# Kernel tuning notes

Measured on AMD Instinct MI355X. Metric: run time of the kernel, lower is better.

## Reference

```python
import jax, jax.numpy as jnp
import numpy as np

B, S = 64, 512
VOCAB, D, H, NH = 50000, 256, 256, 4
MAX_DUR = 12.0
SCALE_RATE = 1.0


def setup_inputs() -> dict:
    key = jax.random.key(0)
    ks = jax.random.split(key, 12)
    s = 1.0 / np.sqrt(H)
    inp = {
        "src": jax.random.randint(ks[0], (B, S), 0, VOCAB),
        "input_len": jax.random.randint(ks[1], (B,), 1, S + 1),
        "fix_src": jax.random.uniform(ks[2], (B, S), jnp.float32) * MAX_DUR,
        "emb_table": jax.random.normal(ks[3], (VOCAB, D), jnp.float32) * 0.02,
        "Wi": jax.random.uniform(ks[4], (H, D), jnp.float32, -s, s),
        "bi": jax.random.uniform(ks[5], (H,), jnp.float32, -s, s),
        "Wh": jax.random.uniform(ks[6], (H, NH * H), jnp.float32, -s, s),
        "bh": jax.random.uniform(ks[7], (H,), jnp.float32, -s, s),
        "fc1_W": jax.random.uniform(ks[8], (D, NH * H), jnp.float32, -s, s),
        "fc1_b": jax.random.uniform(ks[9], (D,), jnp.float32, -s, s),
        "fc2_W": jax.random.uniform(ks[10], (2, D), jnp.float32, -s, s),
        "fc2_b": jax.random.uniform(ks[11], (2,), jnp.float32, -s, s),
    }
    return inp


def _forward(src, input_len, fix_src, emb_table, Wi, bi, Wh, bh, fc1_W, fc1_b, fc2_W, fc2_b):
    emb = emb_table[src]                      # [B, S, D]
    offsets = jnp.arange(NH, dtype=emb.dtype) * (MAX_DUR / NH)  # [NH]
    h0 = jnp.zeros((NH, B, H), emb.dtype)

    def step(h, xd):
        x, d = xd                             # x [B,D], d [B]
        hcat = jnp.swapaxes(h, 0, 1).reshape(B, NH * H)
        cand = jnp.tanh(x @ Wi.T + bi + hcat @ Wh.T + bh)        # [B,H]
        g = jax.nn.sigmoid(d[:, None] * SCALE_RATE - offsets)    # [B,NH]
        gt = g.T[:, :, None]                                     # [NH,B,1]
        h_new = gt * cand[None, :, :] + (1.0 - gt) * h           # [NH,B,H]
        out = jnp.swapaxes(h_new, 0, 1).reshape(B, NH * H)
        return h_new, out

    xs = (jnp.swapaxes(emb, 0, 1), fix_src.T)  # [S,B,D], [S,B]
    _, outs = jax.lax.scan(step, h0, xs)       # [S, B, NH*H]
    outs = jnp.swapaxes(outs, 0, 1)            # [B, S, NH*H]
    sel = outs[jnp.arange(B), input_len - 1]   # gather at last valid step, [B, NH*H]
    hid = jnp.tanh(sel @ fc1_W.T + fc1_b)      # [B, D]
    return hid @ fc2_W.T + fc2_b               # [B, 2]


def reference(src, input_len, fix_src, emb_table, Wi, bi, Wh, bh, fc1_W, fc1_b, fc2_W, fc2_b):
    return _forward(src, input_len, fix_src, emb_table, Wi, bi, Wh, bh, fc1_W, fc1_b, fc2_W, fc2_b)
```

## Files before the change

### kernel.cpp

```cpp
#include <hip/hip_runtime.h>
#include <stdint.h>

constexpr int BB = 64;
constexpr int SS = 512;
constexpr int DD = 256;
constexpr int HH = 256;
constexpr int NHH = 4;
constexpr int KK = 1024;

constexpr int TT = 512;

typedef _Float16 f16;
typedef _Float16 f16x2 __attribute__((ext_vector_type(2)));
typedef _Float16 half8 __attribute__((ext_vector_type(8)));
typedef float f32x4 __attribute__((ext_vector_type(4)));

__device__ inline float dot2p(uint32_t a, uint32_t b, float c) {
  f16x2 av = __builtin_bit_cast(f16x2, a);
  f16x2 bv = __builtin_bit_cast(f16x2, b);
#if defined(__has_builtin)
#if __has_builtin(__builtin_amdgcn_fdot2)
  return __builtin_amdgcn_fdot2(av, bv, c, false);
#else
  return c + (float)av.x * (float)bv.x + (float)av.y * (float)bv.y;
#endif
#else
  return c + (float)av.x * (float)bv.x + (float)av.y * (float)bv.y;
#endif
}

__device__ inline float dot8(uint4 w, uint4 a, float c) {
  c = dot2p(w.x, a.x, c);
  c = dot2p(w.y, a.y, c);
  c = dot2p(w.z, a.z, c);
  c = dot2p(w.w, a.w, c);
  return c;
}

__device__ inline uint32_t pack2(float a, float b) {
  f16x2 v;
  v.x = (f16)a;
  v.y = (f16)b;
  return __builtin_bit_cast(uint32_t, v);
}

__device__ inline float fast_tanh(float x) {
  x = fminf(fmaxf(x, -15.f), 15.f);
  float e = __expf(2.f * x);
  return 1.f - 2.f / (e + 1.f);
}

__device__ __host__ inline int chunk_of(int p, int wv) {
  if (wv == 0) return 2 * p;
  if (wv == 7) return 2 * p + 1;
  return (2 * p + 1 + wv) & 7;
}

__global__ __launch_bounds__(256) void k_prep(
    const float* __restrict__ Wh, uint4* __restrict__ Wq,
    const float* __restrict__ fc1_W, float* __restrict__ fc1T,
    const float* __restrict__ Wi, f16* __restrict__ wif) {
  __shared__ __align__(16) char sarena[16384];
  const int blk = blockIdx.x;
  const int t = threadIdx.x;
  if (blk < 32) {
    f16* lds = (f16*)sarena;
    const int p = blk >> 3, wv = blk & 7;
    const int cw = chunk_of(p, wv);
    {
      const int r = t >> 2, j = t & 3;
      const float* s = Wh + (size_t)(64 * p + r) * KK + 256 * j + 32 * cw;
      f16* d = lds + r * 128 + 32 * j;
#pragma unroll
      for (int i = 0; i < 32; i += 4) {
        float4 x = *(const float4*)(s + i);
        d[i] = (f16)x.x;
        d[i + 1] = (f16)x.y;
        d[i + 2] = (f16)x.z;
        d[i + 3] = (f16)x.w;
      }
    }
    __syncthreads();
    {
      const int mgrp = t >> 6, l = t & 63;
#pragma unroll
      for (int k2 = 0; k2 < 4; ++k2) {
        int mm = mgrp * 4 + k2;
        int j = mm >> 2, u = mm & 3;
        uint4 v = *(const uint4*)(lds + l * 128 + 32 * j + 8 * u);
        Wq[(size_t)(p * 16 + mm) * TT + wv * 64 + l] = v;
      }
    }
  } else if (blk < 288) {
    float* tile = (float*)sarena;
    const int tile_id = blk - 32;
    const int ti = tile_id >> 5, tj = tile_id & 31;
    const int lr = t >> 3, lc4 = t & 7;
    {
      float4 x = *(const float4*)(fc1_W + (size_t)(ti * 32 + lr) * 1024 +
                                  tj * 32 + 4 * lc4);
      float* d = tile + lr * 33 + 4 * lc4;
      d[0] = x.x;
      d[1] = x.y;
      d[2] = x.z;
      d[3] = x.w;
    }
    __syncthreads();
    {
      float4 o;
      o.x = tile[(4 * lc4 + 0) * 33 + lr];
      o.y = tile[(4 * lc4 + 1) * 33 + lr];
      o.z = tile[(4 * lc4 + 2) * 33 + lr];
      o.w = tile[(4 * lc4 + 3) * 33 + lr];
      *(float4*)(fc1T + (size_t)(tj * 32 + lr) * 256 + ti * 32 + 4 * lc4) = o;
    }
  } else {
    const int g4 = ((blk - 288) * 256 + t) * 4;
    float4 x = *(const float4*)(Wi + g4);
    uint2 dw;
    dw.x = pack2(x.x, x.y);
    dw.y = pack2(x.z, x.w);
    *(uint2*)(wif + g4) = dw;
  }
}

__global__ __launch_bounds__(256) void k_u_mfma(
    const int* __restrict__ src, const float* __restrict__ emb,
    const f16* __restrict__ wif, const float* __restrict__ bi,
    const float* __restrict__ bh, const int* __restrict__ input_len,
    f16* __restrict__ U) {
  __shared__ __align__(16) char xls[32768];
  const int row0 = blockIdx.x * 64;
  const int b = row0 >> 9;
  if ((row0 & 511) >= input_len[b]) return;
  const int t = threadIdx.x;
  const int w = t >> 6, l = t & 63;

  for (int rr = 0; rr < 16; ++rr) {
    int r = w * 16 + rr;
    int srcid = src[row0 + r];
    const float4 x = *(const float4*)(emb + (size_t)srcid * DD + l * 4);
    uint2 dw;
    dw.x = pack2(x.x, x.y);
    dw.y = pack2(x.z, x.w);
    int byte = (r * 512 + l * 8) ^ ((r & 7) << 4);
    *(uint2*)(xls + byte) = dw;
  }
  __syncthreads();

  const int lm = l & 15, lk = l >> 4;
  const int arow = w * 16 + lm;
  const int xs = (arow & 7) << 4;

  for (int ct = 0; ct < 16; ++ct) {
    const int o = ct * 16 + lm;
    f32x4 acc = {0.f, 0.f, 0.f, 0.f};
    const f16* bp = wif + (size_t)o * 256 + lk * 8;
#pragma unroll
    for (int kt = 0; kt < 8; ++kt) {
      int ab = (arow * 512 + kt * 64 + lk * 16) ^ xs;
      half8 af = *(const half8*)(xls + ab);
      half8 bf = *(const half8*)(bp + kt * 32);
      acc = __builtin_amdgcn_mfma_f32_16x16x32_f16(af, bf, acc, 0, 0, 0);
    }
    float bias = bi[o] + bh[o];
#pragma unroll
    for (int reg = 0; reg < 4; ++reg) {
      int grow = row0 + w * 16 + lk * 4 + reg;
      U[(size_t)grow * HH + o] = (f16)(acc[reg] + bias);
    }
  }
}

__global__ void __attribute__((amdgpu_flat_work_group_size(512, 512),
                               amdgpu_waves_per_eu(2, 2)))
k_recurrence(
    const uint4* __restrict__ Wq, const f16* __restrict__ U,
    const float* __restrict__ fix_src, const int* __restrict__ input_len,
    const float* __restrict__ fc1T, const float* __restrict__ fc1_b,
    const float* __restrict__ fc2_W, const float* __restrict__ fc2_b,
    float* __restrict__ out, uint32_t* __restrict__ Cex,
    float* __restrict__ FPg, int* __restrict__ Flg) {
  __shared__ __align__(16) char arena[61440];
  f16* cbufX = (f16*)arena;
  uint4* cvecX = (uint4*)arena;
  float* part = (float*)(arena + 512);
  float* partials = (float*)(arena + 512);
  float* hbuf = (float*)(arena + 16896);
  float* fsbuf = (float*)(arena + 17920);

  const int idx = blockIdx.x;
  const int b = idx & 63;
  const int p = idx >> 6;
  const int t = threadIdx.x;
  const int wv = t >> 6, l = t & 63;
  const int out_i = t & 255, ch2 = t >> 8;

  const int cw = chunk_of(p, wv);
  const int q = cw >> 1, half = cw & 1;

  uint4 w[16];
  {
    const uint4* wp = Wq + (p * 16) * TT + t;
#pragma unroll
    for (int m = 0; m < 16; ++m) {
      const uint4* a = wp + m * TT;
      asm volatile("global_load_dwordx4 %0, %1, off"
                   : "=v"(w[m]) : "v"(a) : "memory");
    }
    asm volatile("s_waitcnt vmcnt(0)" ::: "memory");
  }

  float v0 = 0.f, v1 = 0.f, v2 = 0.f, v3 = 0.f;
  float h0 = 0.f, h1 = 0.f, h2 = 0.f, h3 = 0.f;
  float cprev = 0.f, unew = 0.f;

  const int len = input_len[b];
  const f16* Ub = U + (size_t)b * SS * HH;
  const float* fsb = fix_src + b * SS;

  fsbuf[t] = fsb[t];
  if (wv == 0) {
    float c0 = fast_tanh((float)Ub[64 * p + l]);
    f16 chv = (f16)c0;
    cprev = (float)chv;
    if (l < 32) cbufX[2 * p * 32 + l] = chv;
    uint32_t dwp =
        ((uint32_t)__builtin_bit_cast(unsigned short, chv) << 16) | 1u;
    __hip_atomic_store(&Cex[b * 256 + p * 64 + l], dwp, __ATOMIC_RELAXED,
                       __HIP_MEMORY_SCOPE_AGENT);
  }
  __syncthreads();

#pragma unroll 1
  for (int s = 0; s < len; ++s) {
#pragma unroll
    for (int m = 0; m < 16; ++m)
      asm volatile("" : "+v"(w[m].x), "+v"(w[m].y), "+v"(w[m].z), "+v"(w[m].w));

    const int par = s & 1;
    const uint32_t tag = (uint32_t)((s + 1) & 0xffff);
    float g0 = 0.f, g1 = 0.f, g2 = 0.f, g3 = 0.f;

    if (wv == 0) {
      const float dval = fsbuf[s];
      g0 = 1.f / (1.f + __expf(0.f - dval));
      g1 = 1.f / (1.f + __expf(3.f - dval));
      g2 = 1.f / (1.f + __expf(6.f - dval));
      g3 = 1.f / (1.f + __expf(9.f - dval));
      h0 = g0 * cprev + (1.f - g0) * h0;
      h1 = g1 * cprev + (1.f - g1) * h1;
      h2 = g2 * cprev + (1.f - g2) * h2;
      h3 = g3 * cprev + (1.f - g3) * h3;
      int sn = (s + 1 < len) ? (s + 1) : s;
      unew = (float)Ub[(size_t)sn * HH + 64 * p + l];
    } else {
      if (l < 32) {
        uint32_t* addr = &Cex[((par * 64 + b) * 4 + q) * 64 + 32 * half + l];
        uint32_t dw;
        do {
          dw = __hip_atomic_load(addr, __ATOMIC_RELAXED,
                                 __HIP_MEMORY_SCOPE_AGENT);
        } while ((dw & 0xffffu) != tag);
        cbufX[cw * 32 + l] = __builtin_bit_cast(f16, (unsigned short)(dw >> 16));
      }
    }

    {
      const uint4* ap = cvecX + cw * 4;
      uint4 a0 = ap[0], a1 = ap[1], a2 = ap[2], a3 = ap[3];
      float ac0 = 0.f, ac1 = 0.f, ac2 = 0.f, ac3 = 0.f;
      ac0 = dot8(w[0], a0, ac0);  ac0 = dot8(w[1], a1, ac0);
      ac0 = dot8(w[2], a2, ac0);  ac0 = dot8(w[3], a3, ac0);
      ac1 = dot8(w[4], a0, ac1);  ac1 = dot8(w[5], a1, ac1);
      ac1 = dot8(w[6], a2, ac1);  ac1 = dot8(w[7], a3, ac1);
      ac2 = dot8(w[8], a0, ac2);  ac2 = dot8(w[9], a1, ac2);
      ac2 = dot8(w[10], a2, ac2); ac2 = dot8(w[11], a3, ac2);
      ac3 = dot8(w[12], a0, ac3); ac3 = dot8(w[13], a1, ac3);
      ac3 = dot8(w[14], a2, ac3); ac3 = dot8(w[15], a3, ac3);
      float* pr = part + par * 2048 + cw * 256;
      pr[l] = ac0;
      pr[64 + l] = ac1;
      pr[128 + l] = ac2;
      pr[192 + l] = ac3;
    }
    __syncthreads();

    if (wv == 0) {
      float s0 = 0.f, s1 = 0.f, s2 = 0.f, s3 = 0.f;
      const float* pb = part + par * 2048;
#pragma unroll
      for (int kc = 0; kc < 8; ++kc) {
        const float* pr = pb + kc * 256;
        s0 += pr[l];
        s1 += pr[64 + l];
        s2 += pr[128 + l];
        s3 += pr[192 + l];
      }
      v0 = g0 * s0 + (1.f - g0) * v0;
      v1 = g1 * s1 + (1.f - g1) * v1;
      v2 = g2 * s2 + (1.f - g2) * v2;
      v3 = g3 * s3 + (1.f - g3) * v3;
      float c = fast_tanh(unew + (v0 + v1 + v2 + v3));
      f16 chv = (f16)c;
      cprev = (float)chv;
      uint32_t dwp =
          ((uint32_t)__builtin_bit_cast(unsigned short, chv) << 16) |
          (uint32_t)((s + 2) & 0xffff);
      __hip_atomic_store(&Cex[(((s + 1) & 1) * 64 + b) * 256 + p * 64 + l],
                         dwp, __ATOMIC_RELAXED, __HIP_MEMORY_SCOPE_AGENT);
      if (l < 32) cbufX[2 * p * 32 + l] = chv;
    }
  }

  if (wv == 0) {
    hbuf[l] = h0;
    hbuf[64 + l] = h1;
    hbuf[128 + l] = h2;
    hbuf[192 + l] = h3;
  }
  __syncthreads();
  {
    float acc = 0.f;
#pragma unroll 4
    for (int r = 0; r < 128; ++r) {
      int k_loc = ch2 * 128 + r;
      int n2 = k_loc >> 6, il = k_loc & 63;
      int kg = n2 * 256 + 64 * p + il;
      acc += hbuf[k_loc] * fc1T[(size_t)kg * 256 + out_i];
    }
    partials[t] = acc;
  }
  __syncthreads();
  if (t < 256) FPg[(b * 4 + p) * 256 + out_i] =
      partials[out_i] + partials[256 + out_i];
  __syncthreads();
  if (t == 0)
    __hip_atomic_store(&Flg[b * 4 + p], 0x5A5A5A5A, __ATOMIC_RELEASE,
                       __HIP_MEMORY_SCOPE_AGENT);
  if (p != 0) return;
  if (t < 4 && t > 0) {
    while (__hip_atomic_load(&Flg[b * 4 + t], __ATOMIC_ACQUIRE,
                             __HIP_MEMORY_SCOPE_AGENT) != 0x5A5A5A5A) {
    }
  }
  __syncthreads();
  if (t < 256) {
    float pre = fc1_b[t];
#pragma unroll
    for (int qq = 0; qq < 4; ++qq)
      pre += __hip_atomic_load(&FPg[(b * 4 + qq) * 256 + t], __ATOMIC_RELAXED,
                               __HIP_MEMORY_SCOPE_AGENT);
    hbuf[t] = fast_tanh(pre);
  }
  __syncthreads();
  if (t < 64) {
    float p0 = 0.f, p1 = 0.f;
    for (int oi = t; oi < 256; oi += 64) {
      float hh = hbuf[oi];
      p0 += hh * fc2_W[oi];
      p1 += hh * fc2_W[256 + oi];
    }
#pragma unroll
    for (int off = 32; off; off >>= 1) {
      p0 += __shfl_down(p0, off);
      p1 += __shfl_down(p1, off);
    }
    if (t == 0) {
      out[b * 2 + 0] = p0 + fc2_b[0];
      out[b * 2 + 1] = p1 + fc2_b[1];
    }
  }
}

extern "C" void kernel_launch(void* const* d_in, const int* in_sizes, int n_in,
                              void* d_out, int out_size, void* d_ws, size_t ws_size,
                              hipStream_t stream) {
  const int* src = (const int*)d_in[0];
  const int* input_len = (const int*)d_in[1];
  const float* fix_src = (const float*)d_in[2];
  const float* emb = (const float*)d_in[3];
  const float* Wi = (const float*)d_in[4];
  const float* bi = (const float*)d_in[5];
  const float* Wh = (const float*)d_in[6];
  const float* bh = (const float*)d_in[7];
  const float* fc1_W = (const float*)d_in[8];
  const float* fc1_b = (const float*)d_in[9];
  const float* fc2_W = (const float*)d_in[10];
  const float* fc2_b = (const float*)d_in[11];
  float* out = (float*)d_out;

  char* ws = (char*)d_ws;
  uint4* Wq = (uint4*)(ws);
  f16* wif = (f16*)(ws + (512ull << 10));
  float* fc1T = (float*)(ws + (768ull << 10));
  f16* U = (f16*)(ws + (1792ull << 10));
  uint32_t* Cex = (uint32_t*)(ws + (18176ull << 10));
  float* FPg = (float*)(ws + (18304ull << 10));
  int* Flg = (int*)(ws + (18560ull << 10));
  const size_t needed = (18561ull << 10);
  if (ws_size < needed) return;

  k_prep<<<352, 256, 0, stream>>>(Wh, Wq, fc1_W, fc1T, Wi, wif);
  k_u_mfma<<<BB * SS / 64, 256, 0, stream>>>(src, emb, wif, bi, bh,
                                             input_len, U);
  k_recurrence<<<BB * 4, TT, 0, stream>>>(Wq, U, fix_src, input_len, fc1T,
                                          fc1_b, fc2_W, fc2_b, out, Cex, FPg,
                                          Flg);
}
```

Measured before the change: 700.7 us.

## Fuse input projection GEMM into recurrence kernel prologue

Removes the separate k_u_mfma launch. Each recurrence block now computes its own 64-column slice of the input projection U for its batch row, covering only the valid timesteps, before the recurrence starts. This saves a kernel launch and the boundary between the two kernels. In exchange, the 256 recurrence blocks do the GEMM with only 4 of 8 waves active and re-gather the embeddings redundantly across the 4 blocks of each batch. U is still written to global memory and read back afterwards.

```diff
diff --git a/kernel.cpp b/kernel.cpp
--- a/kernel.cpp
+++ b/kernel.cpp
@@ -124,63 +124,18 @@
   }
 }
 
-__global__ __launch_bounds__(256) void k_u_mfma(
-    const int* __restrict__ src, const float* __restrict__ emb,
-    const f16* __restrict__ wif, const float* __restrict__ bi,
-    const float* __restrict__ bh, const int* __restrict__ input_len,
-    f16* __restrict__ U) {
-  __shared__ __align__(16) char xls[32768];
-  const int row0 = blockIdx.x * 64;
-  const int b = row0 >> 9;
-  if ((row0 & 511) >= input_len[b]) return;
-  const int t = threadIdx.x;
-  const int w = t >> 6, l = t & 63;
-
-  for (int rr = 0; rr < 16; ++rr) {
-    int r = w * 16 + rr;
-    int srcid = src[row0 + r];
-    const float4 x = *(const float4*)(emb + (size_t)srcid * DD + l * 4);
-    uint2 dw;
-    dw.x = pack2(x.x, x.y);
-    dw.y = pack2(x.z, x.w);
-    int byte = (r * 512 + l * 8) ^ ((r & 7) << 4);
-    *(uint2*)(xls + byte) = dw;
-  }
-  __syncthreads();
-
-  const int lm = l & 15, lk = l >> 4;
-  const int arow = w * 16 + lm;
-  const int xs = (arow & 7) << 4;
-
-  for (int ct = 0; ct < 16; ++ct) {
-    const int o = ct * 16 + lm;
-    f32x4 acc = {0.f, 0.f, 0.f, 0.f};
-    const f16* bp = wif + (size_t)o * 256 + lk * 8;
-#pragma unroll
-    for (int kt = 0; kt < 8; ++kt) {
-      int ab = (arow * 512 + kt * 64 + lk * 16) ^ xs;
-      half8 af = *(const half8*)(xls + ab);
-      half8 bf = *(const half8*)(bp + kt * 32);
-      acc = __builtin_amdgcn_mfma_f32_16x16x32_f16(af, bf, acc, 0, 0, 0);
-    }
-    float bias = bi[o] + bh[o];
-#pragma unroll
-    for (int reg = 0; reg < 4; ++reg) {
-      int grow = row0 + w * 16 + lk * 4 + reg;
-      U[(size_t)grow * HH + o] = (f16)(acc[reg] + bias);
-    }
-  }
-}
-
 __global__ void __attribute__((amdgpu_flat_work_group_size(512, 512),
                                amdgpu_waves_per_eu(2, 2)))
 k_recurrence(
-    const uint4* __restrict__ Wq, const f16* __restrict__ U,
-    const float* __restrict__ fix_src, const int* __restrict__ input_len,
-    const float* __restrict__ fc1T, const float* __restrict__ fc1_b,
-    const float* __restrict__ fc2_W, const float* __restrict__ fc2_b,
-    float* __restrict__ out, uint32_t* __restrict__ Cex,
-    float* __restrict__ FPg, int* __restrict__ Flg) {
+    const uint4* __restrict__ Wq, const f16* __restrict__ wif,
+    const int* __restrict__ src, const float* __restrict__ emb,
+    const float* __restrict__ bi, const float* __restrict__ bh,
+    f16* __restrict__ U, const float* __restrict__ fix_src,
+    const int* __restrict__ input_len, const float* __restrict__ fc1T,
+    const float* __restrict__ fc1_b, const float* __restrict__ fc2_W,
+    const float* __restrict__ fc2_b, float* __restrict__ out,
+    uint32_t* __restrict__ Cex, float* __restrict__ FPg,
+    int* __restrict__ Flg) {
   __shared__ __align__(16) char arena[61440];
   f16* cbufX = (f16*)arena;
   uint4* cvecX = (uint4*)arena;
@@ -199,6 +154,53 @@
   const int cw = chunk_of(p, wv);
   const int q = cw >> 1, half = cw & 1;
 
+  const int len = input_len[b];
+  const f16* Ub = U + (size_t)b * SS * HH;
+  const float* fsb = fix_src + b * SS;
+
+  {
+    char* xls = arena;
+    const int lm = l & 15, lk = l >> 4;
+    for (int ch = 0; ch < 8; ++ch) {
+      const int row0 = ch * 64;
+      if (row0 >= len) break;
+      for (int rr = 0; rr < 8; ++rr) {
+        int r = wv * 8 + rr;
+        int srcid = src[b * SS + row0 + r];
+        const float4 x = *(const float4*)(emb + (size_t)srcid * DD + l * 4);
+        uint2 dw2;
+        dw2.x = pack2(x.x, x.y);
+        dw2.y = pack2(x.z, x.w);
+        int byte = (r * 512 + l * 8) ^ ((r & 7) << 4);
+        *(uint2*)(xls + byte) = dw2;
+      }
+      __syncthreads();
+      if (wv < 4) {
+        const int arow = wv * 16 + lm;
+        const int xs2 = (arow & 7) << 4;
+        for (int ct = 0; ct < 4; ++ct) {
+          const int o = 64 * p + ct * 16 + lm;
+          f32x4 acc = {0.f, 0.f, 0.f, 0.f};
+          const f16* bp = wif + (size_t)o * 256 + lk * 8;
+#pragma unroll
+          for (int kt = 0; kt < 8; ++kt) {
+            int ab = (arow * 512 + kt * 64 + lk * 16) ^ xs2;
+            half8 af = *(const half8*)(xls + ab);
+            half8 bf = *(const half8*)(bp + kt * 32);
+            acc = __builtin_amdgcn_mfma_f32_16x16x32_f16(af, bf, acc, 0, 0, 0);
+          }
+          float bias2 = bi[o] + bh[o];
+#pragma unroll
+          for (int reg = 0; reg < 4; ++reg) {
+            int srow = row0 + wv * 16 + lk * 4 + reg;
+            U[((size_t)b * SS + srow) * HH + o] = (f16)(acc[reg] + bias2);
+          }
+        }
+      }
+      __syncthreads();
+    }
+  }
+
   uint4 w[16];
   {
     const uint4* wp = Wq + (p * 16) * TT + t;
@@ -214,10 +216,6 @@
   float v0 = 0.f, v1 = 0.f, v2 = 0.f, v3 = 0.f;
   float h0 = 0.f, h1 = 0.f, h2 = 0.f, h3 = 0.f;
   float cprev = 0.f, unew = 0.f;
-
-  const int len = input_len[b];
-  const f16* Ub = U + (size_t)b * SS * HH;
-  const float* fsb = fix_src + b * SS;
 
   fsbuf[t] = fsb[t];
   if (wv == 0) {
@@ -402,9 +400,7 @@
   if (ws_size < needed) return;
 
   k_prep<<<352, 256, 0, stream>>>(Wh, Wq, fc1_W, fc1T, Wi, wif);
-  k_u_mfma<<<BB * SS / 64, 256, 0, stream>>>(src, emb, wif, bi, bh,
-                                             input_len, U);
-  k_recurrence<<<BB * 4, TT, 0, stream>>>(Wq, U, fix_src, input_len, fc1T,
-                                          fc1_b, fc2_W, fc2_b, out, Cex, FPg,
-                                          Flg);
-}
+  k_recurrence<<<BB * 4, TT, 0, stream>>>(Wq, wif, src, emb, bi, bh, U,
+                                          fix_src, input_len, fc1T, fc1_b,
+                                          fc2_W, fc2_b, out, Cex, FPg, Flg);
+}
```

Measured after the change: 728.5 us. 1.04x slower.
